# Optimization experiments

Measured on AMD Instinct MI355X. Metric: run time of the kernel, lower is better.

## Reference

```python
import jax, jax.numpy as jnp
import numpy as np
from jax import lax

B, C, L = 64, 768, 197
DEG = 3          # KACN Chebyshev degree
KW = 3           # conv kernel size
EPS = 1e-5       # BatchNorm eps
END_X = 14.0     # RoPE grid width (14x14 patch grid + 1 CLS token)


def _conv1d(x, W):
    # x: (B, Cin, L), W: (Cout, Cin, K); padding=1 keeps length
    return lax.conv_general_dilated(x, W, window_strides=(1,), padding=[(1, 1)],
                                    dimension_numbers=('NCH', 'OIH', 'NCH'))


def _batchnorm(y, scale, bias):
    # training-mode BatchNorm1d: biased stats over (batch, length)
    mean = jnp.mean(y, axis=(0, 2), keepdims=True)
    var = jnp.var(y, axis=(0, 2), keepdims=True)
    return (y - mean) * lax.rsqrt(var + EPS) * scale[None, :, None] + bias[None, :, None]


def _kacn_proj(x, W, scale, bias):
    # KACNConv1DLayer (groups=1): cos(arange(deg+1) * arccos(tanh(x))) basis, conv, BN
    b, c, l = x.shape
    z = jnp.arccos(jnp.tanh(x))[:, :, None, :] * jnp.arange(DEG + 1, dtype=x.dtype)[None, None, :, None]
    z = jnp.cos(z).reshape(b, c * (DEG + 1), l)  # (B, C*(DEG+1), L), channel-major pairing
    return _batchnorm(_conv1d(z, W), scale, bias)


def _rope(t, cosang, sinang):
    # rotate consecutive channel pairs; t: (B, N, C), cos/sin: (N, C//2)
    b, n, c = t.shape
    p = t.reshape(b, n, c // 2, 2)
    a, bb = p[..., 0], p[..., 1]
    ra = a * cosang[None] - bb * sinang[None]
    rb = a * sinang[None] + bb * cosang[None]
    return jnp.stack([ra, rb], axis=-1).reshape(b, n, c)


def reference(x, Wq, Wk, Wv, bnq_s, bnq_b, bnk_s, bnk_b, bnv_s, bnv_b, gamma, freqs, norm_s, norm_b):
    q = _kacn_proj(x, Wq, bnq_s, bnq_b)
    k = _kacn_proj(x, Wk, bnk_s, bnk_b)
    v = _kacn_proj(x, Wv, bnv_s, bnv_b)
    b, c, l = v.shape
    Q = q.transpose(0, 2, 1)  # (B, L, C)
    K = k.transpose(0, 2, 1)
    # mixed 2D RoPE angles (num_heads=1): t_x, t_y over 14x14 grid
    t = jnp.arange(l - 1, dtype=x.dtype)
    tx = jnp.mod(t, END_X)
    ty = jnp.floor(t / END_X)
    ang = tx[:, None] * freqs[0][None, :] + ty[:, None] * freqs[1][None, :]  # (L-1, C//2)
    cosang, sinang = jnp.cos(ang), jnp.sin(ang)
    # token 0 (CLS) is not rotated
    Qr = jnp.concatenate([Q[:, :1], _rope(Q[:, 1:], cosang, sinang)], axis=1)
    Kr = jnp.concatenate([K[:, :1], _rope(K[:, 1:], cosang, sinang)], axis=1)
    energy = jnp.einsum('bic,bjc->bij', Qr, Kr)          # unscaled, as in the module
    att = jax.nn.softmax(energy, axis=-1)
    out = jnp.einsum('bcj,bij->bci', v, att)             # v @ att^T
    return _batchnorm(gamma[0] * x + out, norm_s, norm_b)


def setup_inputs() -> dict:
    key = jax.random.key(0)
    ks = jax.random.split(key, 5)
    std = 1.0 / (C * (DEG + 1) * KW)
    x = jax.random.normal(ks[0], (B, C, L), dtype=jnp.float32)
    Wq = jax.random.normal(ks[1], (C, C * (DEG + 1), KW), dtype=jnp.float32) * std
    Wk = jax.random.normal(ks[2], (C, C * (DEG + 1), KW), dtype=jnp.float32) * std
    Wv = jax.random.normal(ks[3], (C, C * (DEG + 1), KW), dtype=jnp.float32) * std
    ones = jnp.ones((C,), jnp.float32)
    zeros = jnp.zeros((C,), jnp.float32)
    # init_2d_freqs(dim=C, num_heads=1, theta=10, rotate=True).view(2, -1)
    mag = 1.0 / 10.0 ** (np.arange(0, C, 4)[: C // 4].astype(np.float32) / C)
    ang = float(jax.random.uniform(ks[4], ())) * 2.0 * np.pi
    fx = np.concatenate([mag * np.cos(ang), mag * np.cos(np.pi / 2 + ang)])
    fy = np.concatenate([mag * np.sin(ang), mag * np.sin(np.pi / 2 + ang)])
    freqs = jnp.asarray(np.stack([fx, fy], axis=0), dtype=jnp.float32)  # (2, C//2)
    return {"x": x, "Wq": Wq, "Wk": Wk, "Wv": Wv,
            "bnq_s": ones, "bnq_b": zeros, "bnk_s": ones, "bnk_b": zeros,
            "bnv_s": ones, "bnv_b": zeros,
            "gamma": jnp.zeros((1,), jnp.float32), "freqs": freqs,
            "norm_s": ones, "norm_b": zeros}
```

## Files before the change

kernel.cpp:

```cpp
#include <hip/hip_runtime.h>

#define CCH 768
#define LL  197
#define L199 199
#define KC  2304
#define KTOT 6912
#define MK2 1769472
#define NVALID 12736
#define NROW 12608

typedef __bf16 bf16x8 __attribute__((ext_vector_type(8)));
typedef float f32x2 __attribute__((ext_vector_type(2)));
typedef float f32x4 __attribute__((ext_vector_type(4)));
typedef float f32x16 __attribute__((ext_vector_type(16)));

__device__ __forceinline__ unsigned short f2bf(float f) {
  unsigned int u = __float_as_uint(f);
  u += 0x7FFFu + ((u >> 16) & 1u);
  return (unsigned short)(u >> 16);
}
__device__ __forceinline__ float bf2f(unsigned short h) {
  return __uint_as_float(((unsigned int)h) << 16);
}

__global__ void bias_k(const float* __restrict__ Wq, const float* __restrict__ Wk,
                       const float* __restrict__ Wv, float* __restrict__ bias3) {
  int w = (blockIdx.x * 256 + threadIdx.x) >> 6;
  int lane = threadIdx.x & 63;
  if (w >= 9 * 768) return;
  int proj = w / 2304, rem = w % 2304, tap = rem / 768, m = rem % 768;
  const float* W = proj == 0 ? Wq : (proj == 1 ? Wk : Wv);
  float s = 0.f;
  for (int c = lane; c < 768; c += 64) s += W[((size_t)m * 3072 + c * 4) * 3 + tap];
  for (int off = 32; off; off >>= 1) s += __shfl_down(s, off);
  if (lane == 0) bias3[w] = s;
}

__global__ void pack_w3(const float* __restrict__ Wq, const float* __restrict__ Wk,
                        const float* __restrict__ Wv, unsigned short* __restrict__ Apack,
                        size_t pack1_halves) {
  int u = blockIdx.x * 256 + threadIdx.x;
  if (u >= MK2) return;
  int proj = blockIdx.y;
  const float* W = proj == 0 ? Wq : (proj == 1 ? Wk : Wv);
  unsigned short* Ahi = Apack + (size_t)proj * pack1_halves;
  unsigned short* Alo = Ahi + (size_t)768 * KTOT;
  int m = u / KC, kc = u % KC;
  int c = kc / 3, dm1 = kc % 3;
  int ci = c * 4 + dm1 + 1;
  const float* src = W + ((size_t)m * 3072 + ci) * 3;
#pragma unroll
  for (int tap = 0; tap < 3; ++tap) {
    float f = src[tap];
    unsigned short hi = f2bf(f);
    unsigned short lo = f2bf(f - bf2f(hi));
    size_t idx = (size_t)m * KTOT + tap * KC + kc;
    Ahi[idx] = hi;
    Alo[idx] = lo;
  }
}

__global__ void z_kernel(const float* __restrict__ x, unsigned short* __restrict__ Zhi,
                         unsigned short* __restrict__ Zlo) {
  __shared__ float zs[3][32][33];
  int c0 = blockIdx.x * 32, l0 = blockIdx.y * 32, b = blockIdx.z;
  int t = threadIdx.x;
#pragma unroll
  for (int s = 0; s < 4; ++s) {
    int u = t + 256 * s;
    int rc = u >> 5, cl = u & 31;
    float v = 0.f;
    if (l0 + cl < LL) v = x[((size_t)b * CCH + c0 + rc) * LL + l0 + cl];
    float t1 = tanhf(v);
    zs[0][rc][cl] = t1;
    zs[1][rc][cl] = 2.f * t1 * t1 - 1.f;
    zs[2][rc][cl] = t1 * (4.f * t1 * t1 - 3.f);
  }
  __syncthreads();
#pragma unroll
  for (int s = 0; s < 12; ++s) {
    int w = t + 256 * s;
    int rl = w / 96, cc = w % 96;
    if (l0 + rl < LL) {
      int cl2 = cc / 3, dm1 = cc % 3;
      float v = zs[dm1][cl2][rl];
      unsigned short hi = f2bf(v);
      unsigned short lo = f2bf(v - bf2f(hi));
      size_t row = (size_t)b * L199 + 1 + l0 + rl;
      Zhi[row * KC + c0 * 3 + cc] = hi;
      Zlo[row * KC + c0 * 3 + cc] = lo;
    }
  }
}

__global__ void zero_zpad(unsigned short* __restrict__ Zhi, unsigned short* __restrict__ Zlo) {
  int u = blockIdx.x * 256 + threadIdx.x;
  if (u >= 132 * KC) return;
  int rowi = u / KC, c = u % KC;
  size_t r = (rowi < 128) ? ((size_t)(rowi >> 1) * L199 + (size_t)(rowi & 1) * 198)
                          : ((size_t)NVALID + rowi - 128);
  Zhi[r * KC + c] = 0;
  Zlo[r * KC + c] = 0;
}

#define GLL(SRC, DST) \
  __builtin_amdgcn_global_load_lds( \
      (const __attribute__((address_space(1))) void*)(SRC), \
      (__attribute__((address_space(3))) void*)(DST), 16, 0, 0)

__global__ __launch_bounds__(512, 2) void conv_gemm3(const unsigned short* __restrict__ Apack,
                                                     const unsigned short* __restrict__ Zhi,
                                                     const unsigned short* __restrict__ Zlo,
                                                     const float* __restrict__ bias3,
                                                     float* __restrict__ Oqk,
                                                     float* __restrict__ Ov) {
  __shared__ unsigned short lds[2 * 4 * 8192];
  const int bid = blockIdx.x;
  const int xcd = bid & 7, loc = bid >> 3;
  const int wg = (xcd < 2) ? (xcd * 57 + loc) : (114 + (xcd - 2) * 56 + loc);
  const int n_t = wg / 9, rem = wg % 9;
  const int proj = rem / 3, m_t = rem % 3;
  const int m_blk = m_t * 256, n_blk = n_t * 256;
  const unsigned short* Ahi = Apack + (size_t)proj * 2 * 768 * KTOT;
  const unsigned short* Alo = Ahi + (size_t)768 * KTOT;
  const float* bias3p = bias3 + proj * 2304;
  float* Op = (proj == 2) ? Ov : Oqk + (size_t)proj * NROW * CCH;

  const int t = threadIdx.x;
  const int wave = t >> 6, lane = t & 63;
  const int wm = (wave >> 2) * 128, wn = (wave & 3) * 64;
  f32x16 acc[4][2] = {};

  const int lt = ((lane >> 4) & 1) * 512 + (lane >> 5) * 128 + (lane & 15) * 8;
  const int auoff = (wm >> 4) * 512 + lt;
  const int buoff = (wn >> 4) * 512 + lt;

  const int prow = lane & 15;
  const int kch = lane >> 4;
  const unsigned short* srcs[8];
  int doff[8];
#pragma unroll
  for (int j = 0; j < 8; ++j) {
    int u = (wave << 3) + j;
    int tile = u >> 4, p = u & 15;
    doff[j] = tile * 8192 + p * 512;
    int r;
    const unsigned short* g;
    int rs;
    if (tile < 2) {
      r = m_blk + p * 16 + prow;
      g = (tile == 0) ? Ahi : Alo;
      rs = KTOT;
    } else {
      r = n_blk + p * 16 + prow;
      if (r > 12737) r = 12737;
      g = (tile == 2) ? Zhi : Zlo;
      rs = KC;
    }
    srcs[j] = g + (size_t)r * rs + kch * 8;
  }

  const int NIT = KTOT / 32;
#pragma unroll
  for (int j = 0; j < 8; ++j) GLL(srcs[j], lds + doff[j]);
#pragma unroll
  for (int j = 0; j < 6; ++j) GLL(srcs[j] + 32, lds + 32768 + doff[j]);
  asm volatile("s_waitcnt vmcnt(6)\n\ts_barrier" ::: "memory");
  __builtin_amdgcn_sched_barrier(0);

  for (int i = 0; i < NIT; ++i) {
    const unsigned short* lb = lds + ((i & 1) ? 32768 : 0);
    unsigned short* othbuf = lds + ((i & 1) ? 0 : 32768);
    unsigned short* curbuf = lds + ((i & 1) ? 32768 : 0);
    const int koff_prev = 32 * (i + 1);
    const int koff_cur  = 32 * (i + 2);
    const bool stage_prev = (i < NIT - 1);
    const bool stage_cur  = (i < NIT - 2);

    bf16x8 bh[2][2], bl[2][2];
    bf16x8 ah[2], al[2];

#pragma unroll
    for (int ks = 0; ks < 2; ++ks) {
#pragma unroll
      for (int nb = 0; nb < 2; ++nb) {
        bh[nb][ks] = *(const bf16x8*)(lb + 16384 + buoff + nb * 1024 + ks * 256);
        bl[nb][ks] = *(const bf16x8*)(lb + 24576 + buoff + nb * 1024 + ks * 256);
      }
      ah[ks] = *(const bf16x8*)(lb + auoff + ks * 256);
      al[ks] = *(const bf16x8*)(lb + 8192 + auoff + ks * 256);
    }
    if (stage_prev) {
      GLL(srcs[6] + koff_prev, othbuf + doff[6]);
      GLL(srcs[7] + koff_prev, othbuf + doff[7]);
    }
    asm volatile("s_barrier\n\ts_waitcnt lgkmcnt(0)" ::: "memory");
    __builtin_amdgcn_sched_barrier(0);
    __builtin_amdgcn_s_setprio(1);
#pragma unroll
    for (int p = 0; p < 3; ++p)
#pragma unroll
      for (int ks = 0; ks < 2; ++ks)
#pragma unroll
        for (int nb = 0; nb < 2; ++nb) {
          acc[0][nb] = __builtin_amdgcn_mfma_f32_32x32x16_bf16(
              p == 2 ? al[ks] : ah[ks], p == 1 ? bl[nb][ks] : bh[nb][ks], acc[0][nb], 0, 0, 0);
        }
    __builtin_amdgcn_s_setprio(0);
    asm volatile("s_barrier" ::: "memory");
    __builtin_amdgcn_sched_barrier(0);

#define PHASEQ(Q)                                                                 \
    {                                                                             \
      _Pragma("unroll") for (int ks = 0; ks < 2; ++ks) {                          \
        ah[ks] = *(const bf16x8*)(lb + auoff + (Q) * 1024 + ks * 256);            \
        al[ks] = *(const bf16x8*)(lb + 8192 + auoff + (Q) * 1024 + ks * 256);     \
      }                                                                           \
      if (stage_cur) {                                                            \
        GLL(srcs[2 * ((Q) - 1)] + koff_cur, curbuf + doff[2 * ((Q) - 1)]);        \
        GLL(srcs[2 * ((Q) - 1) + 1] + koff_cur, curbuf + doff[2 * ((Q) - 1) + 1]);\
      }                                                                           \
      asm volatile("s_barrier\n\ts_waitcnt lgkmcnt(0)" ::: "memory");             \
      __builtin_amdgcn_sched_barrier(0);                                          \
      __builtin_amdgcn_s_setprio(1);                                              \
      _Pragma("unroll") for (int p = 0; p < 3; ++p)                               \
      _Pragma("unroll") for (int ks = 0; ks < 2; ++ks)                            \
      _Pragma("unroll") for (int nb = 0; nb < 2; ++nb) {                          \
        acc[Q][nb] = __builtin_amdgcn_mfma_f32_32x32x16_bf16(                     \
            p == 2 ? al[ks] : ah[ks], p == 1 ? bl[nb][ks] : bh[nb][ks],           \
            acc[Q][nb], 0, 0, 0);                                                 \
      }                                                                           \
      __builtin_amdgcn_s_setprio(0);                                              \
    }

    PHASEQ(1)
    asm volatile("s_barrier" ::: "memory");
    __builtin_amdgcn_sched_barrier(0);
    PHASEQ(2)
    asm volatile("s_barrier" ::: "memory");
    __builtin_amdgcn_sched_barrier(0);
    PHASEQ(3)
    if (i < NIT - 2) {
      asm volatile("s_waitcnt vmcnt(6)\n\ts_barrier" ::: "memory");
    } else if (i == NIT - 2) {
      asm volatile("s_waitcnt vmcnt(0)\n\ts_barrier" ::: "memory");
    }
    __builtin_amdgcn_sched_barrier(0);
#undef PHASEQ
  }

  int rowarr[2];
  bool val[2], v0[2], v2[2];
#pragma unroll
  for (int nb = 0; nb < 2; ++nb) {
    int n = n_blk + wn + nb * 32 + (lane & 31);
    int b = n / L199, nl = n - b * L199;
    val[nb] = (n < NVALID) && (nl < LL);
    rowarr[nb] = b * LL + nl;
    v0[nb] = (nl == 0);
    v2[nb] = (nl == 196);
  }
#pragma unroll
  for (int mb = 0; mb < 4; ++mb) {
#pragma unroll
    for (int q = 0; q < 4; ++q) {
      int m = m_blk + wm + mb * 32 + q * 8 + (lane >> 5) * 4;
      f32x4 b0 = *(const f32x4*)(bias3p + m);
      f32x4 b1 = *(const f32x4*)(bias3p + 768 + m);
      f32x4 b2 = *(const f32x4*)(bias3p + 1536 + m);
      f32x4 bs = b0 + b1 + b2;
#pragma unroll
      for (int nb = 0; nb < 2; ++nb) {
        if (val[nb]) {
          f32x4 r;
          r[0] = acc[mb][nb][q * 4 + 0];
          r[1] = acc[mb][nb][q * 4 + 1];
          r[2] = acc[mb][nb][q * 4 + 2];
          r[3] = acc[mb][nb][q * 4 + 3];
          r += bs;
          if (v0[nb]) r -= b0;
          if (v2[nb]) r -= b2;
          *(f32x4*)(Op + (size_t)rowarr[nb] * CCH + m) = r;
        }
      }
    }
  }
}

__global__ void zero_f32(float* __restrict__ p, int n) {
  int u = blockIdx.x * 256 + threadIdx.x;
  if (u < n) p[u] = 0.f;
}

__global__ void bn_stats(const float* __restrict__ Oqk, const float* __restrict__ Ov,
                         float* __restrict__ Ssum, float* __restrict__ Ssq) {
  int proj = blockIdx.z;
  int cb = blockIdx.x * 64;
  int rb = blockIdx.y;
  int t = threadIdx.x;
  int ch = cb + (t & 63);
  int phase = t >> 6;
  const float* Op = (proj == 2) ? Ov : Oqk + (size_t)proj * NROW * CCH;
  float s = 0.f, q = 0.f;
  for (int r = rb * 394 + phase; r < rb * 394 + 394; r += 4) {
    float v = Op[(size_t)r * CCH + ch];
    s += v; q += v * v;
  }
  __shared__ float rs[256], rq[256];
  rs[t] = s; rq[t] = q;
  __syncthreads();
  if (t < 64) {
    float S = rs[t] + rs[t + 64] + rs[t + 128] + rs[t + 192];
    float Q = rq[t] + rq[t + 64] + rq[t + 128] + rq[t + 192];
    atomicAdd(&Ssum[proj * CCH + cb + t], S);
    atomicAdd(&Ssq[proj * CCH + cb + t], Q);
  }
}

__global__ void bn_fin(const float* __restrict__ Ssum, const float* __restrict__ Ssq,
                       const float* __restrict__ sq, const float* __restrict__ bq,
                       const float* __restrict__ sk, const float* __restrict__ bk,
                       const float* __restrict__ sv, const float* __restrict__ bv,
                       float* __restrict__ abn) {
  int u = blockIdx.x * 256 + threadIdx.x;
  if (u >= 3 * CCH) return;
  int proj = u / CCH, ch = u % CCH;
  float mean = Ssum[u] / 12608.f;
  float var = Ssq[u] / 12608.f - mean * mean;
  const float* sc = proj == 0 ? sq : (proj == 1 ? sk : sv);
  const float* bi = proj == 0 ? bq : (proj == 1 ? bk : bv);
  float a = sc[ch] * rsqrtf(var + 1e-5f);
  abn[u * 2] = a;
  abn[u * 2 + 1] = bi[ch] - mean * a;
}

__global__ void rope_pack(const float* __restrict__ Oqk, const float* __restrict__ abn,
                          const float* __restrict__ freqs, float* __restrict__ Qr,
                          float* __restrict__ Kr) {
  size_t u = (size_t)blockIdx.x * 256 + threadIdx.x;
  if (u >= 64ull * LL * 384) return;
  int c2 = (int)(u % 384);
  int l = (int)((u / 384) % LL);
  int b = (int)(u / (384ull * LL));
  size_t rowO = ((size_t)b * LL + l) * CCH + 2 * c2;
  const float* Ok = Oqk + (size_t)NROW * CCH;
  float q0 = Oqk[rowO], q1 = Oqk[rowO + 1];
  float k0 = Ok[rowO], k1 = Ok[rowO + 1];
  float aq0 = abn[(2 * c2) * 2],                bq0 = abn[(2 * c2) * 2 + 1];
  float aq1 = abn[(2 * c2 + 1) * 2],            bq1 = abn[(2 * c2 + 1) * 2 + 1];
  float ak0 = abn[(CCH + 2 * c2) * 2],          bk0 = abn[(CCH + 2 * c2) * 2 + 1];
  float ak1 = abn[(CCH + 2 * c2 + 1) * 2],      bk1 = abn[(CCH + 2 * c2 + 1) * 2 + 1];
  q0 = q0 * aq0 + bq0; q1 = q1 * aq1 + bq1;
  k0 = k0 * ak0 + bk0; k1 = k1 * ak1 + bk1;
  if (l > 0) {
    int tt = l - 1;
    float tx = (float)(tt % 14), ty = (float)(tt / 14);
    float ang = tx * freqs[c2] + ty * freqs[384 + c2];
    float sn, cs;
    sincosf(ang, &sn, &cs);
    float r0 = q0 * cs - q1 * sn, r1 = q0 * sn + q1 * cs;
    q0 = r0; q1 = r1;
    r0 = k0 * cs - k1 * sn; r1 = k0 * sn + k1 * cs;
    k0 = r0; k1 = r1;
  }
  size_t rowT = ((size_t)b * LL + l) * CCH + 2 * c2;
  Qr[rowT] = q0; Qr[rowT + 1] = q1;
  Kr[rowT] = k0; Kr[rowT + 1] = k1;
}

__global__ void energy_k(const float* __restrict__ Qr, const float* __restrict__ Kr,
                         float* __restrict__ E) {
  __shared__ float Qs[64][33], Ks[64][33];
  int i0 = blockIdx.x * 64, j0 = blockIdx.y * 64, b = blockIdx.z;
  int t = threadIdx.x, tj = t & 15, ti = t >> 4;
  float acc[4][4] = {};
  const float* Qb = Qr + (size_t)b * LL * CCH;
  const float* Kb = Kr + (size_t)b * LL * CCH;
  for (int k0 = 0; k0 < CCH; k0 += 32) {
    __syncthreads();
#pragma unroll
    for (int s = 0; s < 8; ++s) {
      int u = t + 256 * s, r = u >> 5, cc = u & 31;
      Qs[r][cc] = (i0 + r < LL) ? Qb[(size_t)(i0 + r) * CCH + k0 + cc] : 0.f;
      Ks[r][cc] = (j0 + r < LL) ? Kb[(size_t)(j0 + r) * CCH + k0 + cc] : 0.f;
    }
    __syncthreads();
#pragma unroll
    for (int kk = 0; kk < 32; ++kk) {
      float qv[4], kv[4];
#pragma unroll
      for (int q = 0; q < 4; ++q) qv[q] = Qs[ti * 4 + q][kk];
#pragma unroll
      for (int j = 0; j < 4; ++j) kv[j] = Ks[tj * 4 + j][kk];
#pragma unroll
      for (int q = 0; q < 4; ++q)
#pragma unroll
        for (int j = 0; j < 4; ++j) acc[q][j] += qv[q] * kv[j];
    }
  }
#pragma unroll
  for (int q = 0; q < 4; ++q) {
    int i = i0 + ti * 4 + q;
    if (i >= LL) continue;
#pragma unroll
    for (int j = 0; j < 4; ++j) {
      int jj = j0 + tj * 4 + j;
      if (jj < LL) E[((size_t)b * LL + i) * LL + jj] = acc[q][j];
    }
  }
}

__global__ void softmax_k(float* __restrict__ E) {
  int row = blockIdx.x;
  int lane = threadIdx.x;
  float* Er = E + (size_t)row * LL;
  float v[4];
  float m = -3.4e38f;
#pragma unroll
  for (int q = 0; q < 4; ++q) {
    int j = lane + 64 * q;
    v[q] = (j < LL) ? Er[j] : -3.4e38f;
    m = fmaxf(m, v[q]);
  }
  for (int off = 32; off; off >>= 1) m = fmaxf(m, __shfl_down(m, off));
  m = __shfl(m, 0);
  float s = 0.f;
#pragma unroll
  for (int q = 0; q < 4; ++q) {
    int j = lane + 64 * q;
    v[q] = (j < LL) ? expf(v[q] - m) : 0.f;
    s += v[q];
  }
  for (int off = 32; off; off >>= 1) s += __shfl_down(s, off);
  s = __shfl(s, 0);
  float inv = 1.f / s;
#pragma unroll
  for (int q = 0; q < 4; ++q) {
    int j = lane + 64 * q;
    if (j < LL) Er[j] = v[q] * inv;
  }
}

__global__ void av_k(const float* __restrict__ att, const float* __restrict__ Ov,
                     const float* __restrict__ abn, float* __restrict__ OA) {
  __shared__ float As[32][33];
  __shared__ float Vs[32][128];
  int i0 = blockIdx.x * 32, c0 = blockIdx.y * 128, b = blockIdx.z;
  int t = threadIdx.x, tc = t & 63, tq = t >> 6;
  const float* attb = att + (size_t)b * LL * LL;
  float acc[8][2] = {};
  for (int j0 = 0; j0 < LL; j0 += 32) {
    __syncthreads();
#pragma unroll
    for (int s = 0; s < 4; ++s) {
      int u = t + 256 * s, r = u >> 5, cc = u & 31;
      As[r][cc] = (i0 + r < LL && j0 + cc < LL) ? attb[(size_t)(i0 + r) * LL + j0 + cc] : 0.f;
    }
#pragma unroll
    for (int s = 0; s < 16; ++s) {
      int u = t + 256 * s, r = u >> 7, cc = u & 127;
      Vs[r][cc] = (j0 + r < LL) ? Ov[((size_t)b * LL + j0 + r) * CCH + c0 + cc] : 0.f;
    }
    __syncthreads();
#pragma unroll
    for (int jj = 0; jj < 32; ++jj) {
      f32x2 vv = *(const f32x2*)&Vs[jj][2 * tc];
#pragma unroll
      for (int q = 0; q < 8; ++q) {
        float a = As[tq * 8 + q][jj];
        acc[q][0] += a * vv[0];
        acc[q][1] += a * vv[1];
      }
    }
  }
  int c = c0 + 2 * tc;
  float a0 = abn[(2 * CCH + c) * 2],     b0 = abn[(2 * CCH + c) * 2 + 1];
  float a1 = abn[(2 * CCH + c + 1) * 2], b1 = abn[(2 * CCH + c + 1) * 2 + 1];
#pragma unroll
  for (int q = 0; q < 8; ++q) {
    int i = i0 + tq * 8 + q;
    if (i < LL) {
      f32x2 r;
      r[0] = a0 * acc[q][0] + b0;
      r[1] = a1 * acc[q][1] + b1;
      *(f32x2*)(OA + ((size_t)b * LL + i) * CCH + c) = r;
    }
  }
}

__global__ void trans_y(const float* __restrict__ OA, const float* __restrict__ x,
                        const float* __restrict__ gamma, float* __restrict__ Y) {
  __shared__ float Ts[32][33];
  int l0 = blockIdx.x * 32, c0 = blockIdx.y * 32, b = blockIdx.z;
  int t = threadIdx.x;
  float g = gamma[0];
#pragma unroll
  for (int s = 0; s < 4; ++s) {
    int u = t + 256 * s, r = u >> 5, cc = u & 31;
    Ts[r][cc] = (l0 + r < LL) ? OA[((size_t)b * LL + l0 + r) * CCH + c0 + cc] : 0.f;
  }
  __syncthreads();
#pragma unroll
  for (int s = 0; s < 4; ++s) {
    int u = t + 256 * s, rc = u >> 5, cl = u & 31;
    if (l0 + cl < LL) {
      size_t idx = ((size_t)b * CCH + c0 + rc) * LL + l0 + cl;
      Y[idx] = g * x[idx] + Ts[cl][rc];
    }
  }
}

__global__ void bn_y(const float* __restrict__ Y, const float* __restrict__ ns,
                     const float* __restrict__ nb, float* __restrict__ fab) {
  int c = blockIdx.x;
  int t = threadIdx.x;
  float s = 0.f, q = 0.f;
  for (int u = t; u < 12608; u += 256) {
    int b = u / LL, l = u % LL;
    float v = Y[((size_t)b * CCH + c) * LL + l];
    s += v; q += v * v;
  }
  __shared__ float rs[256], rq[256];
  rs[t] = s; rq[t] = q;
  __syncthreads();
  for (int off = 128; off; off >>= 1) {
    if (t < off) { rs[t] += rs[t + off]; rq[t] += rq[t + off]; }
    __syncthreads();
  }
  if (t == 0) {
    float mean = rs[0] / 12608.f, var = rq[0] / 12608.f - mean * mean;
    float a = ns[c] * rsqrtf(var + 1e-5f);
    fab[c * 2] = a;
    fab[c * 2 + 1] = nb[c] - mean * a;
  }
}

__global__ void final_k(const float* __restrict__ Y, const float* __restrict__ fab,
                        float* __restrict__ out) {
  size_t u = (size_t)blockIdx.x * 256 + threadIdx.x;
  if (u >= 64ull * CCH * LL) return;
  int c = (int)((u / LL) % CCH);
  out[u] = fab[c * 2] * Y[u] + fab[c * 2 + 1];
}

extern "C" void kernel_launch(void* const* d_in, const int* in_sizes, int n_in,
                              void* d_out, int out_size, void* d_ws, size_t ws_size,
                              hipStream_t stream) {
  const float* x = (const float*)d_in[0];
  const float* Wq = (const float*)d_in[1];
  const float* Wk = (const float*)d_in[2];
  const float* Wv = (const float*)d_in[3];
  const float* bnq_s = (const float*)d_in[4];
  const float* bnq_b = (const float*)d_in[5];
  const float* bnk_s = (const float*)d_in[6];
  const float* bnk_b = (const float*)d_in[7];
  const float* bnv_s = (const float*)d_in[8];
  const float* bnv_b = (const float*)d_in[9];
  const float* gamma = (const float*)d_in[10];
  const float* freqs = (const float*)d_in[11];
  const float* norm_s = (const float*)d_in[12];
  const float* norm_b = (const float*)d_in[13];
  float* out = (float*)d_out;

  char* ws = (char*)d_ws;
  const size_t QRSZ  = 38731776;
  const size_t PACK1 = 21233664;
  const size_t ZSZ   = 58705920;

  const size_t OFS_PACK = 0;
  const size_t OFS_Z    = 3 * PACK1;
  const size_t OFS_ZLO  = OFS_Z + ZSZ;
  const size_t OFS_O    = OFS_ZLO + ZSZ;
  const size_t OFS_MISC = OFS_O + 2 * QRSZ;

  unsigned short* Apack = (unsigned short*)(ws + OFS_PACK);
  unsigned short* Zhi = (unsigned short*)(ws + OFS_Z);
  unsigned short* Zlo = (unsigned short*)(ws + OFS_ZLO);
  float* Oqk = (float*)(ws + OFS_O);
  float* bias3 = (float*)(ws + OFS_MISC);
  float* Ssum = (float*)(ws + OFS_MISC + 27648);
  float* Ssq  = (float*)(ws + OFS_MISC + 36864);
  float* abn  = (float*)(ws + OFS_MISC + 46080);
  float* fab  = (float*)(ws + OFS_MISC + 64512);
  float* Ov = out;
  float* Qr = (float*)(ws + OFS_Z);
  float* Kr = (float*)(ws + OFS_Z + QRSZ);
  float* E  = (float*)(ws + OFS_Z + 2 * QRSZ);
  float* OA = (float*)(ws + OFS_Z);
  float* Y  = (float*)(ws + OFS_Z + QRSZ);

  bias_k<<<dim3(1728), 256, 0, stream>>>(Wq, Wk, Wv, bias3);
  zero_zpad<<<dim3((132 * KC + 255) / 256), 256, 0, stream>>>(Zhi, Zlo);
  z_kernel<<<dim3(24, 7, 64), 256, 0, stream>>>(x, Zhi, Zlo);
  pack_w3<<<dim3((MK2 + 255) / 256, 3), 256, 0, stream>>>(Wq, Wk, Wv, Apack, PACK1 / 2);
  conv_gemm3<<<dim3(450), 512, 0, stream>>>(Apack, Zhi, Zlo, bias3, Oqk, Ov);

  zero_f32<<<dim3(18), 256, 0, stream>>>(Ssum, 4608);
  bn_stats<<<dim3(12, 32, 3), 256, 0, stream>>>(Oqk, Ov, Ssum, Ssq);
  bn_fin<<<dim3(9), 256, 0, stream>>>(Ssum, Ssq, bnq_s, bnq_b, bnk_s, bnk_b, bnv_s, bnv_b, abn);
  rope_pack<<<dim3((unsigned)((64ull * LL * 384 + 255) / 256)), 256, 0, stream>>>(Oqk, abn, freqs, Qr, Kr);
  energy_k<<<dim3(4, 4, 64), 256, 0, stream>>>(Qr, Kr, E);
  softmax_k<<<dim3(64 * LL), 64, 0, stream>>>(E);
  av_k<<<dim3(7, 6, 64), 256, 0, stream>>>(E, Ov, abn, OA);
  trans_y<<<dim3(7, 24, 64), 256, 0, stream>>>(OA, x, gamma, Y);
  bn_y<<<dim3(CCH), 256, 0, stream>>>(Y, norm_s, norm_b, fab);
  final_k<<<dim3((unsigned)((64ull * CCH * LL + 255) / 256)), 256, 0, stream>>>(Y, fab, out);
}
```

Baseline: 1.862 ms.

## Fuse weight packing with bias sums, AV with transpose, and BN stats with output

After: 1.890 ms (median of 2 runs). About the same (+1.5%).

```diff
diff --git a/kernel.cpp b/kernel.cpp
--- a/kernel.cpp
+++ b/kernel.cpp
@@ -23,40 +23,56 @@
   return __uint_as_float(((unsigned int)h) << 16);
 }
 
-__global__ void bias_k(const float* __restrict__ Wq, const float* __restrict__ Wk,
-                       const float* __restrict__ Wv, float* __restrict__ bias3) {
-  int w = (blockIdx.x * 256 + threadIdx.x) >> 6;
-  int lane = threadIdx.x & 63;
-  if (w >= 9 * 768) return;
-  int proj = w / 2304, rem = w % 2304, tap = rem / 768, m = rem % 768;
+__global__ void pack_bias(const float* __restrict__ Wq, const float* __restrict__ Wk,
+                          const float* __restrict__ Wv, unsigned short* __restrict__ Apack,
+                          float* __restrict__ bias3, size_t pack1_halves) {
+  __shared__ float wrow[9216];
+  __shared__ float red0[256], red1[256], red2[256];
+  const int bid = blockIdx.x;
+  const int proj = bid / 768, m = bid % 768;
+  const int t = threadIdx.x;
   const float* W = proj == 0 ? Wq : (proj == 1 ? Wk : Wv);
-  float s = 0.f;
-  for (int c = lane; c < 768; c += 64) s += W[((size_t)m * 3072 + c * 4) * 3 + tap];
-  for (int off = 32; off; off >>= 1) s += __shfl_down(s, off);
-  if (lane == 0) bias3[w] = s;
-}
-
-__global__ void pack_w3(const float* __restrict__ Wq, const float* __restrict__ Wk,
-                        const float* __restrict__ Wv, unsigned short* __restrict__ Apack,
-                        size_t pack1_halves) {
-  int u = blockIdx.x * 256 + threadIdx.x;
-  if (u >= MK2) return;
-  int proj = blockIdx.y;
-  const float* W = proj == 0 ? Wq : (proj == 1 ? Wk : Wv);
+  const float* src = W + (size_t)m * 9216;
+#pragma unroll
+  for (int s = 0; s < 36; ++s) wrow[t + 256 * s] = src[t + 256 * s];
+  __syncthreads();
+  float s0 = 0.f, s1 = 0.f, s2 = 0.f;
+  for (int c = t; c < 768; c += 256) {
+    s0 += wrow[12 * c];
+    s1 += wrow[12 * c + 1];
+    s2 += wrow[12 * c + 2];
+  }
+  red0[t] = s0; red1[t] = s1; red2[t] = s2;
   unsigned short* Ahi = Apack + (size_t)proj * pack1_halves;
   unsigned short* Alo = Ahi + (size_t)768 * KTOT;
-  int m = u / KC, kc = u % KC;
-  int c = kc / 3, dm1 = kc % 3;
-  int ci = c * 4 + dm1 + 1;
-  const float* src = W + ((size_t)m * 3072 + ci) * 3;
-#pragma unroll
-  for (int tap = 0; tap < 3; ++tap) {
-    float f = src[tap];
-    unsigned short hi = f2bf(f);
-    unsigned short lo = f2bf(f - bf2f(hi));
-    size_t idx = (size_t)m * KTOT + tap * KC + kc;
-    Ahi[idx] = hi;
-    Alo[idx] = lo;
+#pragma unroll
+  for (int s = 0; s < 9; ++s) {
+    int u = t + 256 * s;
+    int c = u / 3, dm1 = u % 3;
+    int ci = c * 4 + dm1 + 1;
+#pragma unroll
+    for (int tap = 0; tap < 3; ++tap) {
+      float f = wrow[ci * 3 + tap];
+      unsigned short hi = f2bf(f);
+      unsigned short lo = f2bf(f - bf2f(hi));
+      size_t idx = (size_t)m * KTOT + tap * KC + u;
+      Ahi[idx] = hi;
+      Alo[idx] = lo;
+    }
+  }
+  __syncthreads();
+  for (int off = 128; off; off >>= 1) {
+    if (t < off) {
+      red0[t] += red0[t + off];
+      red1[t] += red1[t + off];
+      red2[t] += red2[t + off];
+    }
+    __syncthreads();
+  }
+  if (t == 0) {
+    bias3[proj * 2304 + m] = red0[0];
+    bias3[proj * 2304 + 768 + m] = red1[0];
+    bias3[proj * 2304 + 1536 + m] = red2[0];
   }
 }
 
@@ -441,10 +457,12 @@
   }
 }
 
-__global__ void av_k(const float* __restrict__ att, const float* __restrict__ Ov,
-                     const float* __restrict__ abn, float* __restrict__ OA) {
+__global__ void av_y(const float* __restrict__ att, const float* __restrict__ Ov,
+                     const float* __restrict__ abn, const float* __restrict__ x,
+                     const float* __restrict__ gamma, float* __restrict__ Y) {
   __shared__ float As[32][33];
   __shared__ float Vs[32][128];
+  __shared__ float Ts[32][129];
   int i0 = blockIdx.x * 32, c0 = blockIdx.y * 128, b = blockIdx.z;
   int t = threadIdx.x, tc = t & 63, tq = t >> 6;
   const float* attb = att + (size_t)b * LL * LL;
@@ -478,69 +496,48 @@
   float a1 = abn[(2 * CCH + c + 1) * 2], b1 = abn[(2 * CCH + c + 1) * 2 + 1];
 #pragma unroll
   for (int q = 0; q < 8; ++q) {
-    int i = i0 + tq * 8 + q;
-    if (i < LL) {
-      f32x2 r;
-      r[0] = a0 * acc[q][0] + b0;
-      r[1] = a1 * acc[q][1] + b1;
-      *(f32x2*)(OA + ((size_t)b * LL + i) * CCH + c) = r;
-    }
-  }
-}
-
-__global__ void trans_y(const float* __restrict__ OA, const float* __restrict__ x,
-                        const float* __restrict__ gamma, float* __restrict__ Y) {
-  __shared__ float Ts[32][33];
-  int l0 = blockIdx.x * 32, c0 = blockIdx.y * 32, b = blockIdx.z;
-  int t = threadIdx.x;
+    int il = tq * 8 + q;
+    Ts[il][2 * tc] = a0 * acc[q][0] + b0;
+    Ts[il][2 * tc + 1] = a1 * acc[q][1] + b1;
+  }
+  __syncthreads();
   float g = gamma[0];
 #pragma unroll
-  for (int s = 0; s < 4; ++s) {
-    int u = t + 256 * s, r = u >> 5, cc = u & 31;
-    Ts[r][cc] = (l0 + r < LL) ? OA[((size_t)b * LL + l0 + r) * CCH + c0 + cc] : 0.f;
-  }
-  __syncthreads();
-#pragma unroll
-  for (int s = 0; s < 4; ++s) {
-    int u = t + 256 * s, rc = u >> 5, cl = u & 31;
-    if (l0 + cl < LL) {
-      size_t idx = ((size_t)b * CCH + c0 + rc) * LL + l0 + cl;
-      Y[idx] = g * x[idx] + Ts[cl][rc];
-    }
-  }
-}
-
-__global__ void bn_y(const float* __restrict__ Y, const float* __restrict__ ns,
-                     const float* __restrict__ nb, float* __restrict__ fab) {
+  for (int s = 0; s < 16; ++s) {
+    int u = t + 256 * s, cc = u >> 5, il = u & 31;
+    if (i0 + il < LL) {
+      size_t idx = ((size_t)b * CCH + c0 + cc) * LL + i0 + il;
+      Y[idx] = g * x[idx] + Ts[il][cc];
+    }
+  }
+}
+
+__global__ void bn_y_final(const float* __restrict__ Y, const float* __restrict__ ns,
+                           const float* __restrict__ nb, float* __restrict__ out) {
+  __shared__ float ych[12608];
+  __shared__ float rs[256], rq[256];
   int c = blockIdx.x;
   int t = threadIdx.x;
   float s = 0.f, q = 0.f;
   for (int u = t; u < 12608; u += 256) {
-    int b = u / LL, l = u % LL;
+    int b = u / LL, l = u - b * LL;
     float v = Y[((size_t)b * CCH + c) * LL + l];
+    ych[u] = v;
     s += v; q += v * v;
   }
-  __shared__ float rs[256], rq[256];
   rs[t] = s; rq[t] = q;
   __syncthreads();
   for (int off = 128; off; off >>= 1) {
     if (t < off) { rs[t] += rs[t + off]; rq[t] += rq[t + off]; }
     __syncthreads();
   }
-  if (t == 0) {
-    float mean = rs[0] / 12608.f, var = rq[0] / 12608.f - mean * mean;
-    float a = ns[c] * rsqrtf(var + 1e-5f);
-    fab[c * 2] = a;
-    fab[c * 2 + 1] = nb[c] - mean * a;
-  }
-}
-
-__global__ void final_k(const float* __restrict__ Y, const float* __restrict__ fab,
-                        float* __restrict__ out) {
-  size_t u = (size_t)blockIdx.x * 256 + threadIdx.x;
-  if (u >= 64ull * CCH * LL) return;
-  int c = (int)((u / LL) % CCH);
-  out[u] = fab[c * 2] * Y[u] + fab[c * 2 + 1];
+  float mean = rs[0] / 12608.f, var = rq[0] / 12608.f - mean * mean;
+  float a = ns[c] * rsqrtf(var + 1e-5f);
+  float bb = nb[c] - mean * a;
+  for (int u = t; u < 12608; u += 256) {
+    int b = u / LL, l = u - b * LL;
+    out[((size_t)b * CCH + c) * LL + l] = a * ych[u] + bb;
+  }
 }
 
 extern "C" void kernel_launch(void* const* d_in, const int* in_sizes, int n_in,
@@ -581,18 +578,15 @@
   float* Ssum = (float*)(ws + OFS_MISC + 27648);
   float* Ssq  = (float*)(ws + OFS_MISC + 36864);
   float* abn  = (float*)(ws + OFS_MISC + 46080);
-  float* fab  = (float*)(ws + OFS_MISC + 64512);
   float* Ov = out;
   float* Qr = (float*)(ws + OFS_Z);
   float* Kr = (float*)(ws + OFS_Z + QRSZ);
   float* E  = (float*)(ws + OFS_Z + 2 * QRSZ);
-  float* OA = (float*)(ws + OFS_Z);
   float* Y  = (float*)(ws + OFS_Z + QRSZ);
 
-  bias_k<<<dim3(1728), 256, 0, stream>>>(Wq, Wk, Wv, bias3);
   zero_zpad<<<dim3((132 * KC + 255) / 256), 256, 0, stream>>>(Zhi, Zlo);
   z_kernel<<<dim3(24, 7, 64), 256, 0, stream>>>(x, Zhi, Zlo);
-  pack_w3<<<dim3((MK2 + 255) / 256, 3), 256, 0, stream>>>(Wq, Wk, Wv, Apack, PACK1 / 2);
+  pack_bias<<<dim3(2304), 256, 0, stream>>>(Wq, Wk, Wv, Apack, bias3, PACK1 / 2);
   conv_gemm3<<<dim3(450), 512, 0, stream>>>(Apack, Zhi, Zlo, bias3, Oqk, Ov);
 
   zero_f32<<<dim3(18), 256, 0, stream>>>(Ssum, 4608);
@@ -601,8 +595,6 @@
   rope_pack<<<dim3((unsigned)((64ull * LL * 384 + 255) / 256)), 256, 0, stream>>>(Oqk, abn, freqs, Qr, Kr);
   energy_k<<<dim3(4, 4, 64), 256, 0, stream>>>(Qr, Kr, E);
   softmax_k<<<dim3(64 * LL), 64, 0, stream>>>(E);
-  av_k<<<dim3(7, 6, 64), 256, 0, stream>>>(E, Ov, abn, OA);
-  trans_y<<<dim3(7, 24, 64), 256, 0, stream>>>(OA, x, gamma, Y);
-  bn_y<<<dim3(CCH), 256, 0, stream>>>(Y, norm_s, norm_b, fab);
-  final_k<<<dim3((unsigned)((64ull * CCH * LL + 255) / 256)), 256, 0, stream>>>(Y, fab, out);
-}
+  av_y<<<dim3(7, 6, 64), 256, 0, stream>>>(E, Ov, abn, x, gamma, Y);
+  bn_y_final<<<dim3(CCH), 256, 0, stream>>>(Y, norm_s, norm_b, out);
+}
```
